# Performance work log

Hardware: AMD Instinct MI355X
Metric: run time of the kernel (lower is better)

## Reference

```python
import jax, jax.numpy as jnp
import numpy as np

N = 50000      # num_nodes
R = 12         # num_relations
RL = 2 * R + 1 # relation slots in each RGCN layer
D = 128        # embedding_dim
H = 128        # hidden_layer_size
B = 4          # num_bases
E = 320000     # num_edges


def _xavier(key, shape):
    fan_in, fan_out = shape[-2], shape[-1]
    lim = np.sqrt(6.0 / (fan_in + fan_out)).astype(np.float32)
    return jax.random.uniform(key, shape, jnp.float32, -lim, lim)


def setup_inputs() -> dict:
    key = jax.random.key(0)
    ks = jax.random.split(key, 12)
    edge_index = jax.random.randint(ks[0], (2, E), 0, N)
    edge_type = jax.random.randint(ks[1], (E,), 0, R)
    neg_tail = jax.random.randint(ks[2], (E,), 0, N)  # corrupted tails for BCE loss
    entity_embedding = _xavier(ks[3], (N, D))
    entity_bias = jnp.zeros((1, D), jnp.float32)
    bases1 = _xavier(ks[4], (B, D, H))
    comp1 = _xavier(ks[5], (RL, B))
    bias1 = jnp.zeros((H,), jnp.float32)
    bases2 = _xavier(ks[6], (B, H, D))
    comp2 = _xavier(ks[7], (RL, B))
    bias2 = jnp.zeros((D,), jnp.float32)
    rel_emb = _xavier(ks[8], (R, D))
    return {
        "entity_embedding": entity_embedding, "entity_bias": entity_bias,
        "bases1": bases1, "comp1": comp1, "bias1": bias1,
        "bases2": bases2, "comp2": comp2, "bias2": bias2,
        "rel_emb": rel_emb,
        "edge_index": edge_index, "edge_type": edge_type, "neg_tail": neg_tail,
    }


def rgcn_layer(x, edge_index, edge_type, bases, comp, bias):
    # Basis-decomposed relational conv: W_r = sum_b comp[r,b] * bases[b]
    # Project once through bases, then combine per-edge with comp[edge_type].
    src, dst = edge_index[0], edge_index[1]
    hb = jnp.einsum('ni,bio->nbo', x, bases)            # [N, B, out]
    c = comp[edge_type]                                  # [E, B]
    msg = jnp.einsum('eb,ebo->eo', c, hb[src])           # [E, out]
    n_edges = edge_type.shape[0]
    deg = jax.ops.segment_sum(jnp.ones((n_edges,), x.dtype), dst, num_segments=N)
    agg = jax.ops.segment_sum(msg, dst, num_segments=N)  # scatter-add aggregation
    return agg / jnp.maximum(deg, 1.0)[:, None] + bias


def reference(entity_embedding, entity_bias, bases1, comp1, bias1,
              bases2, comp2, bias2, rel_emb, edge_index, edge_type, neg_tail):
    x = jax.nn.relu(entity_embedding + entity_bias)
    x = jax.nn.relu(rgcn_layer(x, edge_index, edge_type, bases1, comp1, bias1))
    x = rgcn_layer(x, edge_index, edge_type, bases2, comp2, bias2)
    # DistMult decoding over the graph triples (h, r, t)
    h, t = edge_index[0], edge_index[1]
    re = rel_emb[edge_type]                              # [E, D]
    pred_logits = jnp.sum(x[h] * re * x[t], axis=-1)     # [E]
    neg_logits = jnp.sum(x[h] * re * x[neg_tail], axis=-1)
    loss = 0.5 * (jnp.mean(-jax.nn.log_sigmoid(pred_logits))
                  + jnp.mean(-jax.nn.log_sigmoid(-neg_logits)))
    roc_auc = jnp.mean((pred_logits > neg_logits).astype(jnp.float32))
    return pred_logits, loss, roc_auc
```

## Files before the change

kernel.cpp:

```cpp
#include <hip/hip_runtime.h>

typedef unsigned short ushort_t;
typedef __attribute__((ext_vector_type(8))) short short8;
typedef __attribute__((ext_vector_type(4))) short s16x4;
typedef __attribute__((ext_vector_type(4))) float f32x4;

#define N_NODES 50000
#define NBASE   4
#define N_EDGE  320000
#define DM_BLOCKS 2048
#define N_GROUPS (N_EDGE / 8)
#define SCAN_BLOCKS 49
#define LDSB_STRIDE 136

#define C_COMP1 0
#define C_COMP2 100
#define C_BIAS1 200
#define C_BIAS2 328
#define C_REL   456
#define C_EBIAS 1992
#define C_TOTAL 2120

__device__ __forceinline__ float bf2f(ushort_t u) {
    union { unsigned int i; float f; } v; v.i = ((unsigned int)u) << 16; return v.f;
}
__device__ __forceinline__ ushort_t f2bf(float f) {
    union { float f; unsigned int i; } v; v.f = f;
    unsigned int u = v.i;
    u = (u + 0x7FFFu + ((u >> 16) & 1u)) >> 16;
    return (ushort_t)u;
}
__device__ __forceinline__ float readf(const void* p, int i, int isbf) {
    return isbf ? bf2f(((const ushort_t*)p)[i]) : ((const float*)p)[i];
}
__device__ __forceinline__ float softplus(float x) {
    if (x > 20.f) return x;
    if (x < -20.f) return expf(x);
    return log1pf(expf(x));
}

__global__ void k_prep(const ushort_t* __restrict__ emb, int* __restrict__ flag,
                       const void* comp1, const void* comp2, const void* b1, const void* b2,
                       const void* rel, const void* eb, float* __restrict__ canon) {
    __shared__ int cnt;
    if (threadIdx.x == 0) cnt = 0;
    __syncthreads();
    int e = (emb[threadIdx.x] >> 7) & 0xFF;
    if (e >= 100 && e <= 126) atomicAdd(&cnt, 1);
    __syncthreads();
    if (threadIdx.x == 0) *flag = (cnt >= 200) ? 1 : 0;
    __syncthreads();
    int isbf = (cnt >= 200) ? 1 : 0;
    for (int i = threadIdx.x; i < C_TOTAL; i += blockDim.x) {
        float v;
        if      (i < C_COMP2) v = readf(comp1, i - C_COMP1, isbf);
        else if (i < C_BIAS1) v = readf(comp2, i - C_COMP2, isbf);
        else if (i < C_BIAS2) v = readf(b1,    i - C_BIAS1, isbf);
        else if (i < C_REL)   v = readf(b2,    i - C_BIAS2, isbf);
        else if (i < C_EBIAS) v = readf(rel,   i - C_REL,   isbf);
        else                  v = readf(eb,    i - C_EBIAS, isbf);
        canon[i] = v;
    }
}

__global__ void k_init(const void* __restrict__ bases1, ushort_t* __restrict__ btK1,
                       const void* __restrict__ bases2, ushort_t* __restrict__ btK2,
                       const void* __restrict__ emb, const float* __restrict__ canon,
                       ushort_t* __restrict__ x, const int* __restrict__ flag) {
    int isbf = *flag;
    int bid = blockIdx.x;
    if (bid < 512) {
        const void* bases = (bid < 256) ? bases1 : bases2;
        ushort_t* btK = (bid < 256) ? btK1 : btK2;
        int idx = (bid & 255) * 256 + threadIdx.x;
        int b = idx >> 14, i = (idx >> 7) & 127, o = idx & 127;
        btK[(size_t)o * 512 + (b << 7) + i] = f2bf(readf(bases, idx, isbf));
    } else {
        int i = (bid - 512) * 256 + threadIdx.x;
        if (i < N_NODES * 128) {
            float v = readf(emb, i, isbf) + canon[C_EBIAS + (i & 127)];
            x[i] = f2bf(fmaxf(v, 0.f));
        }
    }
}

__global__ void k_cnt(const int* __restrict__ ei, int* __restrict__ cnt) {
    int e = blockIdx.x * blockDim.x + threadIdx.x;
    if (e >= N_EDGE) return;
    atomicAdd(&cnt[ei[N_EDGE + e]], 1);
}

__global__ void k_scan1(const int* __restrict__ cnt, int* __restrict__ ptr,
                        int* __restrict__ bsum) {
    __shared__ int s[1024];
    int t = threadIdx.x;
    int i = blockIdx.x * 1024 + t;
    int v = (i < N_NODES) ? cnt[i] : 0;
    s[t] = v;
    __syncthreads();
    for (int off = 1; off < 1024; off <<= 1) {
        int u = (t >= off) ? s[t - off] : 0;
        __syncthreads();
        s[t] += u;
        __syncthreads();
    }
    if (i < N_NODES) ptr[i] = s[t] - v;
    if (t == 1023) bsum[blockIdx.x] = s[1023];
}

__global__ void k_scan2(const int* __restrict__ bsum, int* __restrict__ boff) {
    int t = threadIdx.x;
    int v = (t < SCAN_BLOCKS) ? bsum[t] : 0;
    int orig = v;
    #pragma unroll
    for (int off = 1; off < 64; off <<= 1) {
        int u = __shfl_up(v, off);
        if (t >= off) v += u;
    }
    boff[t] = v - orig;
}

__global__ void k_scan3(int* __restrict__ ptr, int* __restrict__ cursor,
                        const int* __restrict__ boff) {
    int t = threadIdx.x;
    int i = blockIdx.x * 1024 + t;
    if (i < N_NODES) {
        int p = ptr[i] + boff[blockIdx.x];
        ptr[i] = p;
        cursor[i] = p;
    }
    if (blockIdx.x == 0 && t == 0) ptr[N_NODES] = N_EDGE;
}

__global__ void k_fill(const int* __restrict__ ei, const int* __restrict__ et,
                       int* __restrict__ cursor, unsigned int* __restrict__ packed) {
    int e = blockIdx.x * blockDim.x + threadIdx.x;
    if (e >= N_EDGE) return;
    int dst = ei[N_EDGE + e];
    int pos = atomicAdd(&cursor[dst], 1);
    packed[pos] = (unsigned int)(ei[e] & 0xFFFF) | ((unsigned int)et[e] << 16);
}

__global__ void k_agg2(const ushort_t* __restrict__ x, const int* __restrict__ ptr,
                       const unsigned int* __restrict__ packed, const float* __restrict__ compf,
                       ushort_t* __restrict__ y) {
    __shared__ __align__(16) float sc[100];
    int tid = threadIdx.x;
    for (int i = tid; i < 100; i += 256) sc[i] = compf[i];
    __syncthreads();
    int m = blockIdx.x * 8 + (tid >> 5);
    int li = tid & 31;
    int c0 = li << 2;
    int beg = ptr[m], end = ptr[m + 1];
    float acc[4][4];
    #pragma unroll
    for (int b = 0; b < 4; ++b)
        #pragma unroll
        for (int j = 0; j < 4; ++j) acc[b][j] = 0.f;

    int i = beg;
    for (; i + 4 <= end; i += 4) {
        unsigned int p0 = packed[i], p1 = packed[i + 1];
        unsigned int p2 = packed[i + 2], p3 = packed[i + 3];
        s16x4 w0 = *(const s16x4*)(x + (size_t)(p0 & 0xFFFFu) * 128 + c0);
        s16x4 w1 = *(const s16x4*)(x + (size_t)(p1 & 0xFFFFu) * 128 + c0);
        s16x4 w2 = *(const s16x4*)(x + (size_t)(p2 & 0xFFFFu) * 128 + c0);
        s16x4 w3 = *(const s16x4*)(x + (size_t)(p3 & 0xFFFFu) * 128 + c0);
        f32x4 cc0 = *(const f32x4*)(sc + (p0 >> 16) * 4);
        f32x4 cc1 = *(const f32x4*)(sc + (p1 >> 16) * 4);
        f32x4 cc2 = *(const f32x4*)(sc + (p2 >> 16) * 4);
        f32x4 cc3 = *(const f32x4*)(sc + (p3 >> 16) * 4);
        #pragma unroll
        for (int j = 0; j < 4; ++j) {
            float v = bf2f((ushort_t)((const short*)&w0)[j]);
            acc[0][j] += cc0[0] * v; acc[1][j] += cc0[1] * v;
            acc[2][j] += cc0[2] * v; acc[3][j] += cc0[3] * v;
        }
        #pragma unroll
        for (int j = 0; j < 4; ++j) {
            float v = bf2f((ushort_t)((const short*)&w1)[j]);
            acc[0][j] += cc1[0] * v; acc[1][j] += cc1[1] * v;
            acc[2][j] += cc1[2] * v; acc[3][j] += cc1[3] * v;
        }
        #pragma unroll
        for (int j = 0; j < 4; ++j) {
            float v = bf2f((ushort_t)((const short*)&w2)[j]);
            acc[0][j] += cc2[0] * v; acc[1][j] += cc2[1] * v;
            acc[2][j] += cc2[2] * v; acc[3][j] += cc2[3] * v;
        }
        #pragma unroll
        for (int j = 0; j < 4; ++j) {
            float v = bf2f((ushort_t)((const short*)&w3)[j]);
            acc[0][j] += cc3[0] * v; acc[1][j] += cc3[1] * v;
            acc[2][j] += cc3[2] * v; acc[3][j] += cc3[3] * v;
        }
    }
    for (; i < end; ++i) {
        unsigned int p0 = packed[i];
        s16x4 w0 = *(const s16x4*)(x + (size_t)(p0 & 0xFFFFu) * 128 + c0);
        f32x4 cc0 = *(const f32x4*)(sc + (p0 >> 16) * 4);
        #pragma unroll
        for (int j = 0; j < 4; ++j) {
            float v = bf2f((ushort_t)((const short*)&w0)[j]);
            acc[0][j] += cc0[0] * v; acc[1][j] += cc0[1] * v;
            acc[2][j] += cc0[2] * v; acc[3][j] += cc0[3] * v;
        }
    }
    ushort_t* yrow = y + (size_t)m * 512;
    #pragma unroll
    for (int b = 0; b < 4; ++b) {
        unsigned int lo = (unsigned int)f2bf(acc[b][0]) | ((unsigned int)f2bf(acc[b][1]) << 16);
        unsigned int hi = (unsigned int)f2bf(acc[b][2]) | ((unsigned int)f2bf(acc[b][3]) << 16);
        unsigned int* yp = (unsigned int*)(yrow + (b << 7) + c0);
        yp[0] = lo;
        yp[1] = hi;
    }
}

__global__ __launch_bounds__(256) void
k_gemm512(const ushort_t* __restrict__ y, const ushort_t* __restrict__ btK,
          const int* __restrict__ cnt, const float* __restrict__ canon,
          ushort_t* __restrict__ xout, int cbias, int dorelu) {
    __shared__ ushort_t bs[128 * LDSB_STRIDE];
    int tid = threadIdx.x;
    int lane = tid & 63, w = tid >> 6;
    int r = lane & 15, q = lane >> 4;
    int m0 = blockIdx.x * 128;
    f32x4 acc[2][8] = {};
    int row0 = m0 + w * 32 + r;
    int row1 = row0 + 16;
    int cr0 = (row0 < N_NODES) ? row0 : (N_NODES - 1);
    int cr1 = (row1 < N_NODES) ? row1 : (N_NODES - 1);
    const ushort_t* ar0 = y + (size_t)cr0 * 512;
    const ushort_t* ar1 = y + (size_t)cr1 * 512;

    for (int c = 0; c < 4; ++c) {
        __syncthreads();
        {
            int o = tid >> 4;
            int j = (tid & 15) << 3;
            #pragma unroll
            for (int s = 0; s < 8; ++s, o += 16) {
                short8 v = *(const short8*)(btK + (size_t)o * 512 + c * 128 + j);
                *(short8*)(bs + o * LDSB_STRIDE + j) = v;
            }
        }
        __syncthreads();
        #pragma unroll
        for (int ksl = 0; ksl < 4; ++ksl) {
            int k0 = ksl * 32 + q * 8;
            short8 a0 = *(const short8*)(ar0 + c * 128 + k0);
            short8 a1 = *(const short8*)(ar1 + c * 128 + k0);
            #pragma unroll
            for (int t = 0; t < 8; ++t) {
                short8 b = *(const short8*)(bs + (t * 16 + r) * LDSB_STRIDE + k0);
                acc[0][t] = __builtin_amdgcn_mfma_f32_16x16x32_bf16(a0, b, acc[0][t], 0, 0, 0);
                acc[1][t] = __builtin_amdgcn_mfma_f32_16x16x32_bf16(a1, b, acc[1][t], 0, 0, 0);
            }
        }
    }
    #pragma unroll
    for (int i = 0; i < 2; ++i) {
        int rbase = m0 + w * 32 + i * 16 + (q << 2);
        float d[4];
        #pragma unroll
        for (int ii = 0; ii < 4; ++ii) {
            int rr = rbase + ii;
            d[ii] = fmaxf((float)cnt[(rr < N_NODES) ? rr : (N_NODES - 1)], 1.0f);
        }
        #pragma unroll
        for (int t = 0; t < 8; ++t) {
            int col = t * 16 + r;
            float bb = canon[cbias + col];
            #pragma unroll
            for (int ii = 0; ii < 4; ++ii) {
                int rr = rbase + ii;
                if (rr < N_NODES) {
                    float v = acc[i][t][ii] / d[ii] + bb;
                    if (dorelu) v = fmaxf(v, 0.f);
                    xout[(size_t)rr * 128 + col] = f2bf(v);
                }
            }
        }
    }
}

__global__ void k_distmult8b(const ushort_t* __restrict__ x2, const float* __restrict__ canon,
                             const int* __restrict__ ei, const int* __restrict__ et,
                             const int* __restrict__ neg, float* __restrict__ outp,
                             float* __restrict__ partials) {
    __shared__ float srel[1536];
    int tid = threadIdx.x;
    for (int i = tid; i < 1536; i += 256) srel[i] = canon[C_REL + i];
    __syncthreads();
    int lane = tid & 63;
    int g = lane >> 3;
    int l = lane & 7;
    int w = (blockIdx.x * blockDim.x + tid) >> 6;
    int nw = (DM_BLOCKS * 256) >> 6;
    float aL1 = 0.f, aL2 = 0.f, aA = 0.f;
    for (int gid = w; gid < N_GROUPS; gid += nw) {
        int e = gid * 8 + g;
        int h = ei[e], t = ei[N_EDGE + e], r = et[e], qn = neg[e];
        const ushort_t* ph = x2 + (size_t)h * 128 + l * 16;
        const ushort_t* pt = x2 + (size_t)t * 128 + l * 16;
        const ushort_t* pq = x2 + (size_t)qn * 128 + l * 16;
        const float*    pr = srel + r * 128 + l * 16;
        short8 h0 = *(const short8*)ph, h1 = *(const short8*)(ph + 8);
        short8 t0 = *(const short8*)pt, t1 = *(const short8*)(pt + 8);
        short8 q0 = *(const short8*)pq, q1 = *(const short8*)(pq + 8);
        float sp = 0.f, sn = 0.f;
        #pragma unroll
        for (int j = 0; j < 8; ++j) {
            float hv = bf2f(((const ushort_t*)&h0)[j]) * pr[j];
            sp += hv * bf2f(((const ushort_t*)&t0)[j]);
            sn += hv * bf2f(((const ushort_t*)&q0)[j]);
        }
        #pragma unroll
        for (int j = 0; j < 8; ++j) {
            float hv = bf2f(((const ushort_t*)&h1)[j]) * pr[8 + j];
            sp += hv * bf2f(((const ushort_t*)&t1)[j]);
            sn += hv * bf2f(((const ushort_t*)&q1)[j]);
        }
        sp += __shfl_down(sp, 4); sn += __shfl_down(sn, 4);
        sp += __shfl_down(sp, 2); sn += __shfl_down(sn, 2);
        sp += __shfl_down(sp, 1); sn += __shfl_down(sn, 1);
        if (l == 0) {
            outp[e] = sp;
            aL1 += softplus(-sp);
            aL2 += softplus(sn);
            aA  += (sp > sn) ? 1.0f : 0.0f;
        }
    }
    #pragma unroll
    for (int off = 32; off; off >>= 1) {
        aL1 += __shfl_down(aL1, off);
        aL2 += __shfl_down(aL2, off);
        aA  += __shfl_down(aA,  off);
    }
    __shared__ float s[3][4];
    int wl = tid >> 6;
    if (lane == 0) { s[0][wl] = aL1; s[1][wl] = aL2; s[2][wl] = aA; }
    __syncthreads();
    if (tid == 0) {
        float t0 = 0.f, t1 = 0.f, t2 = 0.f;
        for (int i = 0; i < 4; ++i) { t0 += s[0][i]; t1 += s[1][i]; t2 += s[2][i]; }
        partials[blockIdx.x * 3 + 0] = t0;
        partials[blockIdx.x * 3 + 1] = t1;
        partials[blockIdx.x * 3 + 2] = t2;
    }
}

__global__ void k_final(const float* __restrict__ partials, float* __restrict__ outp) {
    __shared__ float s[3][256];
    int tid = threadIdx.x;
    float t0 = 0.f, t1 = 0.f, t2 = 0.f;
    for (int i = tid; i < DM_BLOCKS; i += 256) {
        t0 += partials[i * 3 + 0];
        t1 += partials[i * 3 + 1];
        t2 += partials[i * 3 + 2];
    }
    s[0][tid] = t0; s[1][tid] = t1; s[2][tid] = t2;
    __syncthreads();
    for (int st = 128; st; st >>= 1) {
        if (tid < st) {
            s[0][tid] += s[0][tid + st];
            s[1][tid] += s[1][tid + st];
            s[2][tid] += s[2][tid + st];
        }
        __syncthreads();
    }
    if (tid == 0) {
        float inv = 1.0f / (float)N_EDGE;
        outp[N_EDGE]     = 0.5f * (s[0][0] * inv + s[1][0] * inv);
        outp[N_EDGE + 1] = s[2][0] * inv;
    }
}

extern "C" void kernel_launch(void* const* d_in, const int* in_sizes, int n_in,
                              void* d_out, int out_size, void* d_ws, size_t ws_size,
                              hipStream_t stream) {
    const void* emb    = d_in[0];
    const void* ebias  = d_in[1];
    const void* bases1 = d_in[2];
    const void* comp1  = d_in[3];
    const void* bias1  = d_in[4];
    const void* bases2 = d_in[5];
    const void* comp2  = d_in[6];
    const void* bias2  = d_in[7];
    const void* rel    = d_in[8];
    const int*  ei     = (const int*)d_in[9];
    const int*  et     = (const int*)d_in[10];
    const int*  neg    = (const int*)d_in[11];
    float*      outp   = (float*)d_out;

    char* ws = (char*)d_ws;
    size_t off = 0;
    auto alloc = [&](size_t bytes) { char* p = ws + off; off += (bytes + 255) & ~(size_t)255; return p; };
    int*          flag   = (int*)alloc(256);
    float*        canon  = (float*)alloc((size_t)C_TOTAL * 4);
    int*          cnt    = (int*)alloc((size_t)N_NODES * 4);
    int*          ptr    = (int*)alloc((size_t)(N_NODES + 1) * 4);
    int*          cursor = (int*)alloc((size_t)N_NODES * 4);
    int*          bsum   = (int*)alloc(SCAN_BLOCKS * 4);
    int*          boff   = (int*)alloc(64 * 4);
    ushort_t*     btK1   = (ushort_t*)alloc((size_t)128 * 512 * 2);
    ushort_t*     btK2   = (ushort_t*)alloc((size_t)128 * 512 * 2);
    float*        part   = (float*)alloc((size_t)DM_BLOCKS * 3 * 4);
    unsigned int* packed = (unsigned int*)alloc((size_t)N_EDGE * 4);
    ushort_t*     x      = (ushort_t*)alloc((size_t)N_NODES * 128 * 2);
    ushort_t*     y      = (ushort_t*)alloc((size_t)N_NODES * 512 * 2);

    k_prep<<<1, 256, 0, stream>>>((const ushort_t*)emb, flag, comp1, comp2, bias1, bias2,
                                  rel, ebias, canon);
    (void)hipMemsetAsync(cnt, 0, (size_t)N_NODES * 4, stream);
    k_cnt<<<N_EDGE / 256, 256, 0, stream>>>(ei, cnt);
    k_scan1<<<SCAN_BLOCKS, 1024, 0, stream>>>(cnt, ptr, bsum);
    k_scan2<<<1, 64, 0, stream>>>(bsum, boff);
    k_scan3<<<SCAN_BLOCKS, 1024, 0, stream>>>(ptr, cursor, boff);
    k_fill<<<N_EDGE / 256, 256, 0, stream>>>(ei, et, cursor, packed);
    k_init<<<512 + (N_NODES * 128 + 255) / 256, 256, 0, stream>>>(
        bases1, btK1, bases2, btK2, emb, canon, x, flag);

    int ggrid = (N_NODES + 127) / 128;

    k_agg2<<<N_NODES / 8, 256, 0, stream>>>(x, ptr, packed, canon + C_COMP1, y);
    k_gemm512<<<ggrid, 256, 0, stream>>>(y, btK1, cnt, canon, x, C_BIAS1, 1);

    k_agg2<<<N_NODES / 8, 256, 0, stream>>>(x, ptr, packed, canon + C_COMP2, y);
    k_gemm512<<<ggrid, 256, 0, stream>>>(y, btK2, cnt, canon, x, C_BIAS2, 0);

    k_distmult8b<<<DM_BLOCKS, 256, 0, stream>>>(x, canon, ei, et, neg, outp, part);
    k_final<<<1, 256, 0, stream>>>(part, outp);
}
```

Before: 274.9 us.

## Fuse per-layer aggregation and basis GEMM into one kernel via LDS tile

Merges the gather-aggregate kernel and the 512-wide basis GEMM into a single kernel per layer. Each block aggregates 32 destination nodes into an LDS tile of shape [32 x 512] and then runs MFMA directly from that tile, with B fragments read from global memory. This removes the global round-trip of the N x 512 intermediate and one launch per layer, and ping-pongs x between two buffers. The cost is larger LDS use per block, which may lower occupancy, and uncached global reads of the weights in the GEMM phase.

```diff
diff --git a/kernel.cpp b/kernel.cpp
--- a/kernel.cpp
+++ b/kernel.cpp
@@ -11,7 +11,8 @@
 #define DM_BLOCKS 2048
 #define N_GROUPS (N_EDGE / 8)
 #define SCAN_BLOCKS 49
-#define LDSB_STRIDE 136
+#define TILE_M  32
+#define YSTRIDE 520
 
 #define C_COMP1 0
 #define C_COMP2 100
@@ -141,145 +142,129 @@
     packed[pos] = (unsigned int)(ei[e] & 0xFFFF) | ((unsigned int)et[e] << 16);
 }
 
-__global__ void k_agg2(const ushort_t* __restrict__ x, const int* __restrict__ ptr,
-                       const unsigned int* __restrict__ packed, const float* __restrict__ compf,
-                       ushort_t* __restrict__ y) {
+__global__ __launch_bounds__(256) void
+k_fused(const ushort_t* __restrict__ x, const int* __restrict__ ptr,
+        const unsigned int* __restrict__ packed, const float* __restrict__ compf,
+        const ushort_t* __restrict__ btK, const int* __restrict__ cnt,
+        const float* __restrict__ canon, ushort_t* __restrict__ xout,
+        int cbias, int dorelu) {
+    __shared__ __align__(16) ushort_t yt[TILE_M * YSTRIDE];
     __shared__ __align__(16) float sc[100];
     int tid = threadIdx.x;
     for (int i = tid; i < 100; i += 256) sc[i] = compf[i];
     __syncthreads();
-    int m = blockIdx.x * 8 + (tid >> 5);
+
+    int m0 = blockIdx.x * TILE_M;
+    int hw = tid >> 5;
     int li = tid & 31;
     int c0 = li << 2;
-    int beg = ptr[m], end = ptr[m + 1];
-    float acc[4][4];
-    #pragma unroll
-    for (int b = 0; b < 4; ++b)
-        #pragma unroll
-        for (int j = 0; j < 4; ++j) acc[b][j] = 0.f;
-
-    int i = beg;
-    for (; i + 4 <= end; i += 4) {
-        unsigned int p0 = packed[i], p1 = packed[i + 1];
-        unsigned int p2 = packed[i + 2], p3 = packed[i + 3];
-        s16x4 w0 = *(const s16x4*)(x + (size_t)(p0 & 0xFFFFu) * 128 + c0);
-        s16x4 w1 = *(const s16x4*)(x + (size_t)(p1 & 0xFFFFu) * 128 + c0);
-        s16x4 w2 = *(const s16x4*)(x + (size_t)(p2 & 0xFFFFu) * 128 + c0);
-        s16x4 w3 = *(const s16x4*)(x + (size_t)(p3 & 0xFFFFu) * 128 + c0);
-        f32x4 cc0 = *(const f32x4*)(sc + (p0 >> 16) * 4);
-        f32x4 cc1 = *(const f32x4*)(sc + (p1 >> 16) * 4);
-        f32x4 cc2 = *(const f32x4*)(sc + (p2 >> 16) * 4);
-        f32x4 cc3 = *(const f32x4*)(sc + (p3 >> 16) * 4);
-        #pragma unroll
-        for (int j = 0; j < 4; ++j) {
-            float v = bf2f((ushort_t)((const short*)&w0)[j]);
-            acc[0][j] += cc0[0] * v; acc[1][j] += cc0[1] * v;
-            acc[2][j] += cc0[2] * v; acc[3][j] += cc0[3] * v;
-        }
-        #pragma unroll
-        for (int j = 0; j < 4; ++j) {
-            float v = bf2f((ushort_t)((const short*)&w1)[j]);
-            acc[0][j] += cc1[0] * v; acc[1][j] += cc1[1] * v;
-            acc[2][j] += cc1[2] * v; acc[3][j] += cc1[3] * v;
-        }
-        #pragma unroll
-        for (int j = 0; j < 4; ++j) {
-            float v = bf2f((ushort_t)((const short*)&w2)[j]);
-            acc[0][j] += cc2[0] * v; acc[1][j] += cc2[1] * v;
-            acc[2][j] += cc2[2] * v; acc[3][j] += cc2[3] * v;
-        }
-        #pragma unroll
-        for (int j = 0; j < 4; ++j) {
-            float v = bf2f((ushort_t)((const short*)&w3)[j]);
-            acc[0][j] += cc3[0] * v; acc[1][j] += cc3[1] * v;
-            acc[2][j] += cc3[2] * v; acc[3][j] += cc3[3] * v;
-        }
-    }
-    for (; i < end; ++i) {
-        unsigned int p0 = packed[i];
-        s16x4 w0 = *(const s16x4*)(x + (size_t)(p0 & 0xFFFFu) * 128 + c0);
-        f32x4 cc0 = *(const f32x4*)(sc + (p0 >> 16) * 4);
-        #pragma unroll
-        for (int j = 0; j < 4; ++j) {
-            float v = bf2f((ushort_t)((const short*)&w0)[j]);
-            acc[0][j] += cc0[0] * v; acc[1][j] += cc0[1] * v;
-            acc[2][j] += cc0[2] * v; acc[3][j] += cc0[3] * v;
-        }
-    }
-    ushort_t* yrow = y + (size_t)m * 512;
-    #pragma unroll
-    for (int b = 0; b < 4; ++b) {
-        unsigned int lo = (unsigned int)f2bf(acc[b][0]) | ((unsigned int)f2bf(acc[b][1]) << 16);
-        unsigned int hi = (unsigned int)f2bf(acc[b][2]) | ((unsigned int)f2bf(acc[b][3]) << 16);
-        unsigned int* yp = (unsigned int*)(yrow + (b << 7) + c0);
-        yp[0] = lo;
-        yp[1] = hi;
-    }
-}
-
-__global__ __launch_bounds__(256) void
-k_gemm512(const ushort_t* __restrict__ y, const ushort_t* __restrict__ btK,
-          const int* __restrict__ cnt, const float* __restrict__ canon,
-          ushort_t* __restrict__ xout, int cbias, int dorelu) {
-    __shared__ ushort_t bs[128 * LDSB_STRIDE];
-    int tid = threadIdx.x;
+
+    for (int j = 0; j < 4; ++j) {
+        int ml = hw * 4 + j;
+        int m = m0 + ml;
+        float acc[4][4];
+        #pragma unroll
+        for (int b = 0; b < 4; ++b)
+            #pragma unroll
+            for (int jj = 0; jj < 4; ++jj) acc[b][jj] = 0.f;
+
+        if (m < N_NODES) {
+            int beg = ptr[m], end = ptr[m + 1];
+            int i = beg;
+            for (; i + 4 <= end; i += 4) {
+                unsigned int p0 = packed[i], p1 = packed[i + 1];
+                unsigned int p2 = packed[i + 2], p3 = packed[i + 3];
+                s16x4 w0 = *(const s16x4*)(x + (size_t)(p0 & 0xFFFFu) * 128 + c0);
+                s16x4 w1 = *(const s16x4*)(x + (size_t)(p1 & 0xFFFFu) * 128 + c0);
+                s16x4 w2 = *(const s16x4*)(x + (size_t)(p2 & 0xFFFFu) * 128 + c0);
+                s16x4 w3 = *(const s16x4*)(x + (size_t)(p3 & 0xFFFFu) * 128 + c0);
+                f32x4 cc0 = *(const f32x4*)(sc + (p0 >> 16) * 4);
+                f32x4 cc1 = *(const f32x4*)(sc + (p1 >> 16) * 4);
+                f32x4 cc2 = *(const f32x4*)(sc + (p2 >> 16) * 4);
+                f32x4 cc3 = *(const f32x4*)(sc + (p3 >> 16) * 4);
+                #pragma unroll
+                for (int jj = 0; jj < 4; ++jj) {
+                    float v = bf2f((ushort_t)((const short*)&w0)[jj]);
+                    acc[0][jj] += cc0[0] * v; acc[1][jj] += cc0[1] * v;
+                    acc[2][jj] += cc0[2] * v; acc[3][jj] += cc0[3] * v;
+                }
+                #pragma unroll
+                for (int jj = 0; jj < 4; ++jj) {
+                    float v = bf2f((ushort_t)((const short*)&w1)[jj]);
+                    acc[0][jj] += cc1[0] * v; acc[1][jj] += cc1[1] * v;
+                    acc[2][jj] += cc1[2] * v; acc[3][jj] += cc1[3] * v;
+                }
+                #pragma unroll
+                for (int jj = 0; jj < 4; ++jj) {
+                    float v = bf2f((ushort_t)((const short*)&w2)[jj]);
+                    acc[0][jj] += cc2[0] * v; acc[1][jj] += cc2[1] * v;
+                    acc[2][jj] += cc2[2] * v; acc[3][jj] += cc2[3] * v;
+                }
+                #pragma unroll
+                for (int jj = 0; jj < 4; ++jj) {
+                    float v = bf2f((ushort_t)((const short*)&w3)[jj]);
+                    acc[0][jj] += cc3[0] * v; acc[1][jj] += cc3[1] * v;
+                    acc[2][jj] += cc3[2] * v; acc[3][jj] += cc3[3] * v;
+                }
+            }
+            for (; i < end; ++i) {
+                unsigned int p0 = packed[i];
+                s16x4 w0 = *(const s16x4*)(x + (size_t)(p0 & 0xFFFFu) * 128 + c0);
+                f32x4 cc0 = *(const f32x4*)(sc + (p0 >> 16) * 4);
+                #pragma unroll
+                for (int jj = 0; jj < 4; ++jj) {
+                    float v = bf2f((ushort_t)((const short*)&w0)[jj]);
+                    acc[0][jj] += cc0[0] * v; acc[1][jj] += cc0[1] * v;
+                    acc[2][jj] += cc0[2] * v; acc[3][jj] += cc0[3] * v;
+                }
+            }
+        }
+        ushort_t* yrow = yt + ml * YSTRIDE;
+        #pragma unroll
+        for (int b = 0; b < 4; ++b) {
+            unsigned int lo = (unsigned int)f2bf(acc[b][0]) | ((unsigned int)f2bf(acc[b][1]) << 16);
+            unsigned int hi = (unsigned int)f2bf(acc[b][2]) | ((unsigned int)f2bf(acc[b][3]) << 16);
+            unsigned int* yp = (unsigned int*)(yrow + (b << 7) + c0);
+            yp[0] = lo;
+            yp[1] = hi;
+        }
+    }
+    __syncthreads();
+
     int lane = tid & 63, w = tid >> 6;
     int r = lane & 15, q = lane >> 4;
-    int m0 = blockIdx.x * 128;
-    f32x4 acc[2][8] = {};
-    int row0 = m0 + w * 32 + r;
-    int row1 = row0 + 16;
-    int cr0 = (row0 < N_NODES) ? row0 : (N_NODES - 1);
-    int cr1 = (row1 < N_NODES) ? row1 : (N_NODES - 1);
-    const ushort_t* ar0 = y + (size_t)cr0 * 512;
-    const ushort_t* ar1 = y + (size_t)cr1 * 512;
-
-    for (int c = 0; c < 4; ++c) {
-        __syncthreads();
-        {
-            int o = tid >> 4;
-            int j = (tid & 15) << 3;
-            #pragma unroll
-            for (int s = 0; s < 8; ++s, o += 16) {
-                short8 v = *(const short8*)(btK + (size_t)o * 512 + c * 128 + j);
-                *(short8*)(bs + o * LDSB_STRIDE + j) = v;
-            }
-        }
-        __syncthreads();
-        #pragma unroll
-        for (int ksl = 0; ksl < 4; ++ksl) {
-            int k0 = ksl * 32 + q * 8;
-            short8 a0 = *(const short8*)(ar0 + c * 128 + k0);
-            short8 a1 = *(const short8*)(ar1 + c * 128 + k0);
-            #pragma unroll
-            for (int t = 0; t < 8; ++t) {
-                short8 b = *(const short8*)(bs + (t * 16 + r) * LDSB_STRIDE + k0);
-                acc[0][t] = __builtin_amdgcn_mfma_f32_16x16x32_bf16(a0, b, acc[0][t], 0, 0, 0);
-                acc[1][t] = __builtin_amdgcn_mfma_f32_16x16x32_bf16(a1, b, acc[1][t], 0, 0, 0);
-            }
-        }
-    }
+    int wr = w & 1, wc = w >> 1;
+    f32x4 gacc[4] = {};
+    const ushort_t* arow = yt + (wr * 16 + r) * YSTRIDE + q * 8;
+    const ushort_t* bbase = btK + (size_t)(wc * 64 + r) * 512 + q * 8;
     #pragma unroll
-    for (int i = 0; i < 2; ++i) {
-        int rbase = m0 + w * 32 + i * 16 + (q << 2);
-        float d[4];
+    for (int step = 0; step < 16; ++step) {
+        short8 a = *(const short8*)(arow + step * 32);
+        #pragma unroll
+        for (int t = 0; t < 4; ++t) {
+            short8 b = *(const short8*)(bbase + t * 16 * 512 + step * 32);
+            gacc[t] = __builtin_amdgcn_mfma_f32_16x16x32_bf16(a, b, gacc[t], 0, 0, 0);
+        }
+    }
+
+    int rbase = m0 + wr * 16 + (q << 2);
+    float d[4];
+    #pragma unroll
+    for (int ii = 0; ii < 4; ++ii) {
+        int rr = rbase + ii;
+        d[ii] = fmaxf((float)cnt[(rr < N_NODES) ? rr : (N_NODES - 1)], 1.0f);
+    }
+    #pragma unroll
+    for (int t = 0; t < 4; ++t) {
+        int col = wc * 64 + t * 16 + r;
+        float bb = canon[cbias + col];
         #pragma unroll
         for (int ii = 0; ii < 4; ++ii) {
             int rr = rbase + ii;
-            d[ii] = fmaxf((float)cnt[(rr < N_NODES) ? rr : (N_NODES - 1)], 1.0f);
-        }
-        #pragma unroll
-        for (int t = 0; t < 8; ++t) {
-            int col = t * 16 + r;
-            float bb = canon[cbias + col];
-            #pragma unroll
-            for (int ii = 0; ii < 4; ++ii) {
-                int rr = rbase + ii;
-                if (rr < N_NODES) {
-                    float v = acc[i][t][ii] / d[ii] + bb;
-                    if (dorelu) v = fmaxf(v, 0.f);
-                    xout[(size_t)rr * 128 + col] = f2bf(v);
-                }
+            if (rr < N_NODES) {
+                float v = gacc[t][ii] / d[ii] + bb;
+                if (dorelu) v = fmaxf(v, 0.f);
+                xout[(size_t)rr * 128 + col] = f2bf(v);
             }
         }
     }
@@ -409,7 +394,7 @@
     float*        part   = (float*)alloc((size_t)DM_BLOCKS * 3 * 4);
     unsigned int* packed = (unsigned int*)alloc((size_t)N_EDGE * 4);
     ushort_t*     x      = (ushort_t*)alloc((size_t)N_NODES * 128 * 2);
-    ushort_t*     y      = (ushort_t*)alloc((size_t)N_NODES * 512 * 2);
+    ushort_t*     xb     = (ushort_t*)alloc((size_t)N_NODES * 128 * 2);
 
     k_prep<<<1, 256, 0, stream>>>((const ushort_t*)emb, flag, comp1, comp2, bias1, bias2,
                                   rel, ebias, canon);
@@ -422,13 +407,12 @@
     k_init<<<512 + (N_NODES * 128 + 255) / 256, 256, 0, stream>>>(
         bases1, btK1, bases2, btK2, emb, canon, x, flag);
 
-    int ggrid = (N_NODES + 127) / 128;
-
-    k_agg2<<<N_NODES / 8, 256, 0, stream>>>(x, ptr, packed, canon + C_COMP1, y);
-    k_gemm512<<<ggrid, 256, 0, stream>>>(y, btK1, cnt, canon, x, C_BIAS1, 1);
-
-    k_agg2<<<N_NODES / 8, 256, 0, stream>>>(x, ptr, packed, canon + C_COMP2, y);
-    k_gemm512<<<ggrid, 256, 0, stream>>>(y, btK2, cnt, canon, x, C_BIAS2, 0);
+    int fgrid = (N_NODES + TILE_M - 1) / TILE_M;
+
+    k_fused<<<fgrid, 256, 0, stream>>>(x, ptr, packed, canon + C_COMP1, btK1, cnt,
+                                       canon, xb, C_BIAS1, 1);
+    k_fused<<<fgrid, 256, 0, stream>>>(xb, ptr, packed, canon + C_COMP2, btK2, cnt,
+                                       canon, x, C_BIAS2, 0);
 
     k_distmult8b<<<DM_BLOCKS, 256, 0, stream>>>(x, canon, ei, et, neg, outp, part);
     k_final<<<1, 256, 0, stream>>>(part, outp);
```

Measured after the change: 345.4 us. 1.26x slower.
